# Optimization experiments

Measured on AMD Instinct MI355X. Metric: run time of the kernel, lower is better.

The kernel has to match this reference:

```python
import jax, jax.numpy as jnp
import numpy as np

B, S, D = 32, 2048, 64
TEMPERATURE = 8.0  # sqrt(d_k)
NEG = -1e10


def setup_inputs() -> dict:
    key = jax.random.key(0)
    kq, kk, kv, kp = jax.random.split(key, 4)
    q = jax.random.normal(kq, (B, S, D), dtype=jnp.float32)
    k = jax.random.normal(kk, (B, S, D), dtype=jnp.float32)
    v = jax.random.normal(kv, (B, S, D), dtype=jnp.float32)
    # attn_mask: causal mask (True = masked out), broadcast to [B,S,S]
    causal = jnp.triu(jnp.ones((S, S), dtype=jnp.bool_), k=1)
    attn_mask = jnp.broadcast_to(causal, (B, S, S))
    # mask: key-padding mask from random lengths (True = padded key)
    lengths = jax.random.randint(kp, (B,), S // 2, S + 1)  # [B]
    key_pad = jnp.arange(S)[None, :] >= lengths[:, None]   # [B,S] True where padded
    mask = jnp.broadcast_to(key_pad[:, None, :], (B, S, S))
    return {"q": q, "k": k, "v": v, "mask": mask, "attn_mask": attn_mask}


def reference(q, k, v, mask, attn_mask):
    # attn = bmm(q, k^T) / temperature  -> [B, S, S]
    attn = jnp.einsum("bqd,bkd->bqk", q, k) / TEMPERATURE
    attn = jnp.where(attn_mask, NEG, attn)
    attn = jnp.where(mask, NEG, attn)
    attn = jax.nn.softmax(attn, axis=2)
    # dropout p=0.0 -> identity
    output = jnp.einsum("bqk,bkd->bqd", attn, v)  # [B, S, D]
    return (output, attn)
```

## Files before the change

### kernel.cpp

```cpp
#include <hip/hip_runtime.h>
#include <stdint.h>

#define BB 32
#define SS 2048
#define DH 64
#define BQ 64
#define BK 64
#define NW 4
#define NQT (SS/BQ)
#define S2 0.18033688f

typedef __attribute__((ext_vector_type(8))) short bf16x8;
typedef __attribute__((ext_vector_type(4))) float f32x4;

#define MFMA(a,b,c) __builtin_amdgcn_mfma_f32_16x16x32_bf16((a),(b),(c),0,0,0)
#define SW(row, d) (((row) << 6) + ((d) ^ (((row) & 7) << 3)))

__device__ __forceinline__ short bf16h(float x) {
  uint32_t u = __float_as_uint(x);
  return (short)((u + 0x7fffu + ((u >> 16) & 1u)) >> 16);
}

__global__ void detect_mask_kernel(const uint32_t* __restrict__ m, int* flag) {
  if (threadIdx.x == 0) *flag = 0;
  __syncthreads();
  int viol = 0;
  for (int i = threadIdx.x; i < 8 * 2048; i += blockDim.x) {
    const int b = i >> 11, k = i & 2047;
    viol |= (m[(size_t)b * SS * SS + k] > 1u);
  }
  if (__ballot(viol) && (threadIdx.x & 63) == 0) atomicOr(flag, 1);
}

__global__ __launch_bounds__(256, 4)
void sdpa_kernel(const float* __restrict__ qg, const float* __restrict__ kg,
                 const float* __restrict__ vg, const void* __restrict__ maskg,
                 const int* __restrict__ mflagp,
                 float* __restrict__ outg, float* __restrict__ attng) {
  __shared__ short kh[BK * DH];
  __shared__ short vth[DH * BK];
  __shared__ short p16[NW * 16 * BK];

  const int tid = threadIdx.x;
  const int w = tid >> 6, l = tid & 63;
  const int ln = l & 15, gr = l >> 4;

  const int b = blockIdx.x & (BB - 1);
  const int qt = (NQT - 1) - (blockIdx.x >> 5);
  const int q0 = qt * BQ;
  const int wr0 = q0 + w * 16;
  const int nct = qt + 1;

  const int mask_is_byte = *mflagp;
  const uint8_t* padu8 = (const uint8_t*)maskg + (size_t)b * SS * SS;
  const int* padi32 = (const int*)maskg + (size_t)b * SS * SS;
  const f32x4 z4 = {0.f, 0.f, 0.f, 0.f};

  bf16x8 qh8[2];
#pragma unroll
  for (int ks = 0; ks < 2; ++ks) {
    const float* qp = qg + (size_t)(b * SS + wr0 + ln) * DH + ks * 32 + gr * 8;
    f32x4 x0 = *(const f32x4*)qp;
    f32x4 x1 = *(const f32x4*)(qp + 4);
#pragma unroll
    for (int j = 0; j < 4; ++j) {
      qh8[ks][j] = bf16h(x0[j]);
      qh8[ks][4 + j] = bf16h(x1[j]);
    }
  }

  {
    const int c0 = nct * BK;
    for (int rr = 0; rr < BQ; ++rr) {
      float* arow = attng + (size_t)(b * SS + q0 + rr) * SS + c0;
      for (int cc = tid * 4; cc < SS - c0; cc += 256 * 4)
        *(f32x4*)(arow + cc) = z4;
    }
  }

  auto stageK = [&](int kt0) {
    const float* base = kg + (size_t)(b * SS + kt0) * DH;
#pragma unroll
    for (int i = 0; i < 4; ++i) {
      const int e = i * 1024 + tid * 4;
      f32x4 x = *(const f32x4*)(base + e);
      const int idx = SW(e >> 6, e & 63);
      *(short4*)&kh[idx] =
          make_short4(bf16h(x[0]), bf16h(x[1]), bf16h(x[2]), bf16h(x[3]));
    }
  };

  auto stageV = [&](int kt0) {
    const int g4 = (tid & 15) << 2, r0 = (tid >> 4) << 2;
    f32x4 x[4];
#pragma unroll
    for (int i = 0; i < 4; ++i)
      x[i] = *(const f32x4*)(vg + (size_t)(b * SS + kt0 + r0 + i) * DH + g4);
#pragma unroll
    for (int dd = 0; dd < 4; ++dd) {
      const int idx = SW(g4 + dd, r0);
      *(short4*)&vth[idx] = make_short4(bf16h(x[0][dd]), bf16h(x[1][dd]),
                                        bf16h(x[2][dd]), bf16h(x[3][dd]));
    }
  };

  auto loadPad = [&](int kt0, bool padk[4]) -> bool {
    bool all = true;
#pragma unroll
    for (int nt = 0; nt < 4; ++nt) {
      const int col = kt0 + nt * 16 + ln;
      padk[nt] = mask_is_byte ? (padu8[col] != 0) : (padi32[col] != 0);
      all = all && padk[nt];
    }
    return __all(all);
  };

  auto qkt = [&](f32x4 acc[4]) {
#pragma unroll
    for (int ks = 0; ks < 2; ++ks)
#pragma unroll
      for (int nt = 0; nt < 4; ++nt) {
        bf16x8 bh = *(const bf16x8*)&kh[SW(nt * 16 + ln, ks * 32 + gr * 8)];
        acc[nt] = MFMA(qh8[ks], bh, acc[nt]);
      }
  };

  float rs[4] = {0.f, 0.f, 0.f, 0.f};
  for (int kt = 0; kt < nct; ++kt) {
    const int kt0 = kt * BK;
    bool padk[4];
    if (loadPad(kt0, padk)) continue;
    stageK(kt0);
    __syncthreads();

    f32x4 acc[4] = {z4, z4, z4, z4};
    qkt(acc);

    const bool needc = (kt0 + BK - 1) > wr0;
    float tmp[4] = {0.f, 0.f, 0.f, 0.f};
#pragma unroll
    for (int nt = 0; nt < 4; ++nt) {
      const int colg = kt0 + nt * 16 + ln;
#pragma unroll
      for (int j = 0; j < 4; ++j) {
        const int rowg = wr0 + gr * 4 + j;
        const bool dead = padk[nt] || (needc && colg > rowg);
        tmp[j] += dead ? 0.f : exp2f(acc[nt][j] * S2);
      }
    }
#pragma unroll
    for (int off = 1; off < 16; off <<= 1)
#pragma unroll
      for (int j = 0; j < 4; ++j) tmp[j] += __shfl_xor(tmp[j], off);
#pragma unroll
    for (int j = 0; j < 4; ++j) rs[j] += tmp[j];
    __syncthreads();
  }

  float rinv[4];
#pragma unroll
  for (int j = 0; j < 4; ++j) rinv[j] = 1.f / rs[j];

  f32x4 oacc[4] = {z4, z4, z4, z4};
  for (int kt = 0; kt < nct; ++kt) {
    const int kt0 = kt * BK;
    bool padk[4];
    if (loadPad(kt0, padk)) {
#pragma unroll
      for (int nt = 0; nt < 4; ++nt)
#pragma unroll
        for (int j = 0; j < 4; ++j)
          attng[(size_t)(b * SS + wr0 + gr * 4 + j) * SS + kt0 + nt * 16 + ln] = 0.f;
      continue;
    }
    stageK(kt0);
    stageV(kt0);
    __syncthreads();

    f32x4 acc[4] = {z4, z4, z4, z4};
    qkt(acc);

    const bool needc = (kt0 + BK - 1) > wr0;
#pragma unroll
    for (int nt = 0; nt < 4; ++nt) {
      const int colg = kt0 + nt * 16 + ln;
#pragma unroll
      for (int j = 0; j < 4; ++j) {
        const int rowg = wr0 + gr * 4 + j;
        const bool dead = padk[nt] || (needc && colg > rowg);
        const float pv = dead ? 0.f : exp2f(acc[nt][j] * S2) * rinv[j];
        attng[(size_t)(b * SS + rowg) * SS + colg] = pv;
        const int prow = gr * 4 + j;
        p16[(w * 16 + prow) * 64 + ((nt * 16 + ln) ^ ((prow & 7) << 3))] =
            bf16h(pv);
      }
    }
#pragma unroll
    for (int ks = 0; ks < 2; ++ks) {
      bf16x8 pa =
          *(const bf16x8*)&p16[(w * 16 + ln) * 64 +
                               ((ks * 32 + gr * 8) ^ ((ln & 7) << 3))];
#pragma unroll
      for (int nt = 0; nt < 4; ++nt) {
        bf16x8 vb = *(const bf16x8*)&vth[SW(nt * 16 + ln, ks * 32 + gr * 8)];
        oacc[nt] = MFMA(pa, vb, oacc[nt]);
      }
    }
    __syncthreads();
  }

#pragma unroll
  for (int nt = 0; nt < 4; ++nt)
#pragma unroll
    for (int j = 0; j < 4; ++j)
      outg[(size_t)(b * SS + wr0 + gr * 4 + j) * DH + nt * 16 + ln] = oacc[nt][j];
}

extern "C" void kernel_launch(void* const* d_in, const int* in_sizes, int n_in,
                              void* d_out, int out_size, void* d_ws, size_t ws_size,
                              hipStream_t stream) {
  const float* q = (const float*)d_in[0];
  const float* k = (const float*)d_in[1];
  const float* v = (const float*)d_in[2];
  const void* mask = d_in[3];
  float* out = (float*)d_out;
  float* attn = out + (size_t)BB * SS * DH;
  int* mflag = (int*)d_ws;

  detect_mask_kernel<<<dim3(1), dim3(1024), 0, stream>>>((const uint32_t*)mask, mflag);
  sdpa_kernel<<<dim3(BB * NQT), dim3(256), 0, stream>>>(q, k, v, mask, mflag, out, attn);
}
```

Measured before the change: 1.163 ms.

## Split key range into chunks across blocks with atomic row-sum and output reduction

```diff
diff --git a/kernel.cpp b/kernel.cpp
--- a/kernel.cpp
+++ b/kernel.cpp
@@ -4,10 +4,11 @@
 #define BB 32
 #define SS 2048
 #define DH 64
-#define BQ 64
 #define BK 64
-#define NW 4
-#define NQT (SS/BQ)
+#define QR 64
+#define NQT (SS/QR)
+#define CHUNK 8
+#define PPB 80
 #define S2 0.18033688f
 
 typedef __attribute__((ext_vector_type(8))) short bf16x8;
@@ -19,6 +20,13 @@
 __device__ __forceinline__ short bf16h(float x) {
   uint32_t u = __float_as_uint(x);
   return (short)((u + 0x7fffu + ((u >> 16) & 1u)) >> 16);
+}
+
+__device__ __forceinline__ void decode_pair(int p, int& qt, int& kc) {
+  if (p < 32)      { qt = 31 - (p >> 2); kc = p & 3; }
+  else if (p < 56) { int u = p - 32, d = u / 3; qt = 23 - d; kc = u - d * 3; }
+  else if (p < 72) { int u = p - 56; qt = 15 - (u >> 1); kc = u & 1; }
+  else             { qt = 7 - (p - 72); kc = 0; }
 }
 
 __global__ void detect_mask_kernel(const uint32_t* __restrict__ m, int* flag) {
@@ -33,23 +41,18 @@
 }
 
 __global__ __launch_bounds__(256, 4)
-void sdpa_kernel(const float* __restrict__ qg, const float* __restrict__ kg,
-                 const float* __restrict__ vg, const void* __restrict__ maskg,
-                 const int* __restrict__ mflagp,
-                 float* __restrict__ outg, float* __restrict__ attng) {
+void sums_kernel(const float* __restrict__ qg, const float* __restrict__ kg,
+                 const void* __restrict__ maskg, const int* __restrict__ mflagp,
+                 float* __restrict__ wsum) {
   __shared__ short kh[BK * DH];
-  __shared__ short vth[DH * BK];
-  __shared__ short p16[NW * 16 * BK];
-
   const int tid = threadIdx.x;
   const int w = tid >> 6, l = tid & 63;
   const int ln = l & 15, gr = l >> 4;
-
   const int b = blockIdx.x & (BB - 1);
-  const int qt = (NQT - 1) - (blockIdx.x >> 5);
-  const int q0 = qt * BQ;
-  const int wr0 = q0 + w * 16;
-  const int nct = qt + 1;
+  int qt, kc; decode_pair(blockIdx.x >> 5, qt, kc);
+  const int ktlo = kc * CHUNK;
+  const int kthi = min(ktlo + CHUNK - 1, qt);
+  const int wr0 = qt * QR + w * 16;
 
   const int mask_is_byte = *mflagp;
   const uint8_t* padu8 = (const uint8_t*)maskg + (size_t)b * SS * SS;
@@ -63,59 +66,34 @@
     f32x4 x0 = *(const f32x4*)qp;
     f32x4 x1 = *(const f32x4*)(qp + 4);
 #pragma unroll
-    for (int j = 0; j < 4; ++j) {
-      qh8[ks][j] = bf16h(x0[j]);
-      qh8[ks][4 + j] = bf16h(x1[j]);
-    }
-  }
-
-  {
-    const int c0 = nct * BK;
-    for (int rr = 0; rr < BQ; ++rr) {
-      float* arow = attng + (size_t)(b * SS + q0 + rr) * SS + c0;
-      for (int cc = tid * 4; cc < SS - c0; cc += 256 * 4)
-        *(f32x4*)(arow + cc) = z4;
-    }
-  }
-
-  auto stageK = [&](int kt0) {
-    const float* base = kg + (size_t)(b * SS + kt0) * DH;
-#pragma unroll
-    for (int i = 0; i < 4; ++i) {
-      const int e = i * 1024 + tid * 4;
-      f32x4 x = *(const f32x4*)(base + e);
-      const int idx = SW(e >> 6, e & 63);
-      *(short4*)&kh[idx] =
-          make_short4(bf16h(x[0]), bf16h(x[1]), bf16h(x[2]), bf16h(x[3]));
-    }
-  };
-
-  auto stageV = [&](int kt0) {
-    const int g4 = (tid & 15) << 2, r0 = (tid >> 4) << 2;
-    f32x4 x[4];
-#pragma unroll
-    for (int i = 0; i < 4; ++i)
-      x[i] = *(const f32x4*)(vg + (size_t)(b * SS + kt0 + r0 + i) * DH + g4);
-#pragma unroll
-    for (int dd = 0; dd < 4; ++dd) {
-      const int idx = SW(g4 + dd, r0);
-      *(short4*)&vth[idx] = make_short4(bf16h(x[0][dd]), bf16h(x[1][dd]),
-                                        bf16h(x[2][dd]), bf16h(x[3][dd]));
-    }
-  };
-
-  auto loadPad = [&](int kt0, bool padk[4]) -> bool {
-    bool all = true;
+    for (int j = 0; j < 4; ++j) { qh8[ks][j] = bf16h(x0[j]); qh8[ks][4+j] = bf16h(x1[j]); }
+  }
+
+  float rs[4] = {0.f, 0.f, 0.f, 0.f};
+  for (int kt = ktlo; kt <= kthi; ++kt) {
+    const int kt0 = kt * BK;
+    bool padk[4]; bool all = true;
 #pragma unroll
     for (int nt = 0; nt < 4; ++nt) {
       const int col = kt0 + nt * 16 + ln;
       padk[nt] = mask_is_byte ? (padu8[col] != 0) : (padi32[col] != 0);
       all = all && padk[nt];
     }
-    return __all(all);
-  };
-
-  auto qkt = [&](f32x4 acc[4]) {
+    if (__all(all)) continue;
+
+    {
+      const float* base = kg + (size_t)(b * SS + kt0) * DH;
+#pragma unroll
+      for (int i = 0; i < 4; ++i) {
+        const int e = i * 1024 + tid * 4;
+        f32x4 x = *(const f32x4*)(base + e);
+        *(short4*)&kh[SW(e >> 6, e & 63)] =
+            make_short4(bf16h(x[0]), bf16h(x[1]), bf16h(x[2]), bf16h(x[3]));
+      }
+    }
+    __syncthreads();
+
+    f32x4 acc[4] = {z4, z4, z4, z4};
 #pragma unroll
     for (int ks = 0; ks < 2; ++ks)
 #pragma unroll
@@ -123,21 +101,8 @@
         bf16x8 bh = *(const bf16x8*)&kh[SW(nt * 16 + ln, ks * 32 + gr * 8)];
         acc[nt] = MFMA(qh8[ks], bh, acc[nt]);
       }
-  };
-
-  float rs[4] = {0.f, 0.f, 0.f, 0.f};
-  for (int kt = 0; kt < nct; ++kt) {
-    const int kt0 = kt * BK;
-    bool padk[4];
-    if (loadPad(kt0, padk)) continue;
-    stageK(kt0);
-    __syncthreads();
-
-    f32x4 acc[4] = {z4, z4, z4, z4};
-    qkt(acc);
 
     const bool needc = (kt0 + BK - 1) > wr0;
-    float tmp[4] = {0.f, 0.f, 0.f, 0.f};
 #pragma unroll
     for (int nt = 0; nt < 4; ++nt) {
       const int colg = kt0 + nt * 16 + ln;
@@ -145,27 +110,79 @@
       for (int j = 0; j < 4; ++j) {
         const int rowg = wr0 + gr * 4 + j;
         const bool dead = padk[nt] || (needc && colg > rowg);
-        tmp[j] += dead ? 0.f : exp2f(acc[nt][j] * S2);
-      }
-    }
-#pragma unroll
-    for (int off = 1; off < 16; off <<= 1)
-#pragma unroll
-      for (int j = 0; j < 4; ++j) tmp[j] += __shfl_xor(tmp[j], off);
-#pragma unroll
-    for (int j = 0; j < 4; ++j) rs[j] += tmp[j];
-    __syncthreads();
-  }
+        rs[j] += dead ? 0.f : exp2f(acc[nt][j] * S2);
+      }
+    }
+    __syncthreads();
+  }
+
+#pragma unroll
+  for (int off = 1; off < 16; off <<= 1)
+#pragma unroll
+    for (int j = 0; j < 4; ++j) rs[j] += __shfl_xor(rs[j], off);
+  if (ln == 0)
+#pragma unroll
+    for (int j = 0; j < 4; ++j)
+      atomicAdd(&wsum[b * SS + wr0 + gr * 4 + j], rs[j]);
+}
+
+__global__ __launch_bounds__(256, 4)
+void attn_pv_kernel(const float* __restrict__ qg, const float* __restrict__ kg,
+                    const float* __restrict__ vg, const void* __restrict__ maskg,
+                    const int* __restrict__ mflagp, const float* __restrict__ wsum,
+                    float* __restrict__ outg, float* __restrict__ attng) {
+  __shared__ short kh[BK * DH];
+  __shared__ short vth[DH * BK];
+  __shared__ short p16[4 * 16 * BK];
+  const int tid = threadIdx.x;
+  const int w = tid >> 6, l = tid & 63;
+  const int ln = l & 15, gr = l >> 4;
+  const int b = blockIdx.x & (BB - 1);
+  int qt, kc; decode_pair(blockIdx.x >> 5, qt, kc);
+  const int ktlo = kc * CHUNK;
+  const int kthi = min(ktlo + CHUNK - 1, qt);
+  const int wr0 = qt * QR + w * 16;
+
+  const int mask_is_byte = *mflagp;
+  const uint8_t* padu8 = (const uint8_t*)maskg + (size_t)b * SS * SS;
+  const int* padi32 = (const int*)maskg + (size_t)b * SS * SS;
+  const f32x4 z4 = {0.f, 0.f, 0.f, 0.f};
 
   float rinv[4];
 #pragma unroll
-  for (int j = 0; j < 4; ++j) rinv[j] = 1.f / rs[j];
+  for (int j = 0; j < 4; ++j)
+    rinv[j] = 1.f / wsum[b * SS + wr0 + gr * 4 + j];
+
+  bf16x8 qh8[2];
+#pragma unroll
+  for (int ks = 0; ks < 2; ++ks) {
+    const float* qp = qg + (size_t)(b * SS + wr0 + ln) * DH + ks * 32 + gr * 8;
+    f32x4 x0 = *(const f32x4*)qp;
+    f32x4 x1 = *(const f32x4*)(qp + 4);
+#pragma unroll
+    for (int j = 0; j < 4; ++j) { qh8[ks][j] = bf16h(x0[j]); qh8[ks][4+j] = bf16h(x1[j]); }
+  }
+
+  if (kc == 0) {
+    const int c0 = (qt + 1) * QR;
+    for (int rr = 0; rr < QR; ++rr) {
+      float* arow = attng + (size_t)(b * SS + qt * QR + rr) * SS + c0;
+      for (int cc = tid * 4; cc < SS - c0; cc += 256 * 4)
+        *(f32x4*)(arow + cc) = z4;
+    }
+  }
 
   f32x4 oacc[4] = {z4, z4, z4, z4};
-  for (int kt = 0; kt < nct; ++kt) {
+  for (int kt = ktlo; kt <= kthi; ++kt) {
     const int kt0 = kt * BK;
-    bool padk[4];
-    if (loadPad(kt0, padk)) {
+    bool padk[4]; bool all = true;
+#pragma unroll
+    for (int nt = 0; nt < 4; ++nt) {
+      const int col = kt0 + nt * 16 + ln;
+      padk[nt] = mask_is_byte ? (padu8[col] != 0) : (padi32[col] != 0);
+      all = all && padk[nt];
+    }
+    if (__all(all)) {
 #pragma unroll
       for (int nt = 0; nt < 4; ++nt)
 #pragma unroll
@@ -173,12 +190,39 @@
           attng[(size_t)(b * SS + wr0 + gr * 4 + j) * SS + kt0 + nt * 16 + ln] = 0.f;
       continue;
     }
-    stageK(kt0);
-    stageV(kt0);
+
+    {
+      const float* base = kg + (size_t)(b * SS + kt0) * DH;
+#pragma unroll
+      for (int i = 0; i < 4; ++i) {
+        const int e = i * 1024 + tid * 4;
+        f32x4 x = *(const f32x4*)(base + e);
+        *(short4*)&kh[SW(e >> 6, e & 63)] =
+            make_short4(bf16h(x[0]), bf16h(x[1]), bf16h(x[2]), bf16h(x[3]));
+      }
+    }
+    {
+      const int g4 = (tid & 15) << 2, r0 = (tid >> 4) << 2;
+      f32x4 x[4];
+#pragma unroll
+      for (int i = 0; i < 4; ++i)
+        x[i] = *(const f32x4*)(vg + (size_t)(b * SS + kt0 + r0 + i) * DH + g4);
+#pragma unroll
+      for (int dd = 0; dd < 4; ++dd)
+        *(short4*)&vth[SW(g4 + dd, r0)] =
+            make_short4(bf16h(x[0][dd]), bf16h(x[1][dd]),
+                        bf16h(x[2][dd]), bf16h(x[3][dd]));
+    }
     __syncthreads();
 
     f32x4 acc[4] = {z4, z4, z4, z4};
-    qkt(acc);
+#pragma unroll
+    for (int ks = 0; ks < 2; ++ks)
+#pragma unroll
+      for (int nt = 0; nt < 4; ++nt) {
+        bf16x8 bh = *(const bf16x8*)&kh[SW(nt * 16 + ln, ks * 32 + gr * 8)];
+        acc[nt] = MFMA(qh8[ks], bh, acc[nt]);
+      }
 
     const bool needc = (kt0 + BK - 1) > wr0;
 #pragma unroll
@@ -191,15 +235,13 @@
         const float pv = dead ? 0.f : exp2f(acc[nt][j] * S2) * rinv[j];
         attng[(size_t)(b * SS + rowg) * SS + colg] = pv;
         const int prow = gr * 4 + j;
-        p16[(w * 16 + prow) * 64 + ((nt * 16 + ln) ^ ((prow & 7) << 3))] =
-            bf16h(pv);
+        p16[(w * 16 + prow) * 64 + ((nt * 16 + ln) ^ ((prow & 7) << 3))] = bf16h(pv);
       }
     }
 #pragma unroll
     for (int ks = 0; ks < 2; ++ks) {
-      bf16x8 pa =
-          *(const bf16x8*)&p16[(w * 16 + ln) * 64 +
-                               ((ks * 32 + gr * 8) ^ ((ln & 7) << 3))];
+      bf16x8 pa = *(const bf16x8*)&p16[(w * 16 + ln) * 64 +
+                                       ((ks * 32 + gr * 8) ^ ((ln & 7) << 3))];
 #pragma unroll
       for (int nt = 0; nt < 4; ++nt) {
         bf16x8 vb = *(const bf16x8*)&vth[SW(nt * 16 + ln, ks * 32 + gr * 8)];
@@ -213,7 +255,8 @@
   for (int nt = 0; nt < 4; ++nt)
 #pragma unroll
     for (int j = 0; j < 4; ++j)
-      outg[(size_t)(b * SS + wr0 + gr * 4 + j) * DH + nt * 16 + ln] = oacc[nt][j];
+      atomicAdd(&outg[(size_t)(b * SS + wr0 + gr * 4 + j) * DH + nt * 16 + ln],
+                oacc[nt][j]);
 }
 
 extern "C" void kernel_launch(void* const* d_in, const int* in_sizes, int n_in,
@@ -226,7 +269,12 @@
   float* out = (float*)d_out;
   float* attn = out + (size_t)BB * SS * DH;
   int* mflag = (int*)d_ws;
+  float* wsum = (float*)((char*)d_ws + 256);
 
   detect_mask_kernel<<<dim3(1), dim3(1024), 0, stream>>>((const uint32_t*)mask, mflag);
-  sdpa_kernel<<<dim3(BB * NQT), dim3(256), 0, stream>>>(q, k, v, mask, mflag, out, attn);
-}
+  hipMemsetAsync(wsum, 0, (size_t)BB * SS * sizeof(float), stream);
+  hipMemsetAsync(out, 0, (size_t)BB * SS * DH * sizeof(float), stream);
+  sums_kernel<<<dim3(BB * PPB), dim3(256), 0, stream>>>(q, k, mask, mflag, wsum);
+  attn_pv_kernel<<<dim3(BB * PPB), dim3(256), 0, stream>>>(q, k, v, mask, mflag,
+                                                           wsum, out, attn);
+}
```

Result: faster. 1.103 ms (-5.1%).
